# Kernel optimization log

Hardware: AMD Instinct MI355X
Metric: run time of the kernel (lower is better)

## Reference

```python
import jax, jax.numpy as jnp
import numpy as np

N = 50000
E = 800000
IN_C, HID_C, OUT_C = 128, 128, 64


def setup_inputs() -> dict:
    key = jax.random.key(0)
    k1, k2, k3, k4 = jax.random.split(key, 4)
    x = jax.random.normal(k1, (N, IN_C), dtype=jnp.float32)
    edge_index = jax.random.randint(k2, (2, E), 0, N, dtype=jnp.int32)
    # Glorot-ish init for the two linear layers (PyG GCNConv uses glorot)
    W1 = jax.random.normal(k3, (IN_C, HID_C), dtype=jnp.float32) / np.sqrt(IN_C)
    b1 = jnp.zeros((HID_C,), dtype=jnp.float32)
    W2 = jax.random.normal(k4, (HID_C, OUT_C), dtype=jnp.float32) / np.sqrt(HID_C)
    b2 = jnp.zeros((OUT_C,), dtype=jnp.float32)
    return {"x": x, "edge_index": edge_index, "W1": W1, "b1": b1, "W2": W2, "b2": b2}


def _gcn_norm(edge_index, num_nodes):
    # Add self-loops, then symmetric normalization deg^{-1/2}[row]*deg^{-1/2}[col]
    loop = jnp.arange(num_nodes, dtype=edge_index.dtype)
    row = jnp.concatenate([edge_index[0], loop])  # [E+N] source
    col = jnp.concatenate([edge_index[1], loop])  # [E+N] destination
    deg = jax.ops.segment_sum(jnp.ones_like(col, dtype=jnp.float32), col,
                              num_segments=num_nodes)
    deg_isqrt = jax.lax.rsqrt(deg)  # deg >= 1 due to self-loops
    norm = deg_isqrt[row] * deg_isqrt[col]  # [E+N]
    return row, col, norm


def _gcn_conv(x, row, col, norm, W, b, num_nodes):
    x = x @ W                                   # [N, C_out]
    msg = x[row] * norm[:, None]                # gather + scale, [E+N, C_out]
    out = jax.ops.segment_sum(msg, col, num_segments=num_nodes)  # scatter-add
    return out + b


def reference(x, edge_index, W1, b1, W2, b2):
    num_nodes = x.shape[0]
    row, col, norm = _gcn_norm(edge_index, num_nodes)
    h = _gcn_conv(x, row, col, norm, W1, b1, num_nodes)
    h = jax.nn.relu(h)
    out = _gcn_conv(h, row, col, norm, W2, b2, num_nodes)
    return out
```

## Files before the change

kernel.cpp:

```cpp
#include <hip/hip_runtime.h>


typedef float f32x4 __attribute__((ext_vector_type(4)));
typedef short bf16x8 __attribute__((ext_vector_type(8)));

#define EPB 4096

__device__ inline float bf2f(unsigned short u) {
    return __uint_as_float(((unsigned int)u) << 16);
}
__device__ inline unsigned short f2bf(float f) {
    unsigned int x = __float_as_uint(f);
    x = x + 0x7FFFu + ((x >> 16) & 1u);
    return (unsigned short)(x >> 16);
}
__device__ inline float4 cvt4(ushort4 u) {
    return make_float4(bf2f(u.x), bf2f(u.y), bf2f(u.z), bf2f(u.w));
}

__global__ __launch_bounds__(256) void k_rhist(const int* __restrict__ col,
                                               int* __restrict__ bbase,
                                               int* __restrict__ bucket_cnt,
                                               const float* __restrict__ W1,
                                               const float* __restrict__ W2,
                                               unsigned short* __restrict__ Wt1,
                                               unsigned short* __restrict__ Wt2,
                                               int e, int nbR, int nbB) {
    if ((int)blockIdx.x >= nbR) {
        int i = ((int)blockIdx.x - nbR) * 256 + threadIdx.x;
        if (i < 16384) {
            int k = i >> 7, nc = i & 127;
            Wt1[nc * 128 + k] = f2bf(W1[i]);
        } else if (i < 24576) {
            int i2 = i - 16384;
            int k = i2 >> 6, nc = i2 & 63;
            Wt2[nc * 128 + k] = f2bf(W2[i2]);
        }
        return;
    }
    __shared__ int h[256];
    int t = threadIdx.x;
    h[t] = 0;
    __syncthreads();
    int base = blockIdx.x * EPB;
#pragma unroll
    for (int i = 0; i < EPB / 256; ++i) {
        int idx = base + t + i * 256;
        if (idx < e) atomicAdd(&h[col[idx] >> 8], 1);
    }
    __syncthreads();
    if (t < nbB) bbase[t * nbR + blockIdx.x] = atomicAdd(&bucket_cnt[t], h[t]);
}

__global__ __launch_bounds__(256) void k_scanB(const int* __restrict__ bucket_cnt,
                                               int* __restrict__ bucket_base, int nbB) {
    __shared__ int s[256];
    int t = threadIdx.x;
    int v = (t < nbB) ? bucket_cnt[t] : 0;
    s[t] = v;
    __syncthreads();
#pragma unroll
    for (int off = 1; off < 256; off <<= 1) {
        int u = (t >= off) ? s[t - off] : 0;
        __syncthreads();
        s[t] += u;
        __syncthreads();
    }
    if (t < nbB) bucket_base[t] = s[t] - v;
    if (t == 255) bucket_base[nbB] = s[255];
}

__global__ __launch_bounds__(256) void k_rscatter(const int* __restrict__ row,
                                                  const int* __restrict__ col,
                                                  const int* __restrict__ bucket_base,
                                                  const int* __restrict__ bbase,
                                                  unsigned int* __restrict__ tmp,
                                                  int e, int nbR, int nbB) {
    __shared__ int base[256];
    __shared__ int h[256];
    int t = threadIdx.x;
    base[t] = (t < nbB) ? bucket_base[t] + bbase[t * nbR + blockIdx.x] : 0;
    h[t] = 0;
    __syncthreads();
    int b0 = blockIdx.x * EPB;
#pragma unroll
    for (int i = 0; i < EPB / 256; ++i) {
        int idx = b0 + t + i * 256;
        if (idx < e) {
            int c = col[idx];
            int bin = c >> 8;
            int rk = atomicAdd(&h[bin], 1);
            tmp[base[bin] + rk] =
                ((unsigned int)(c & 255) << 16) | (unsigned int)row[idx];
        }
    }
}

__global__ __launch_bounds__(256) void k_bsort(const unsigned int* __restrict__ tmp,
                                               const int* __restrict__ bucket_base,
                                               int* __restrict__ indptr,
                                               float* __restrict__ dinv,
                                               unsigned short* __restrict__ srcidx,
                                               int n, int e, int nbB) {
    __shared__ int cnt[256];
    __shared__ int pre[256];
    int b = blockIdx.x;
    int t = threadIdx.x;
    int beg = bucket_base[b];
    int end = bucket_base[b + 1];

    cnt[t] = 0;
    __syncthreads();
    for (int i = beg + t; i < end; i += 256) atomicAdd(&cnt[tmp[i] >> 16], 1);
    __syncthreads();
    int v = cnt[t];
    pre[t] = v;
    __syncthreads();
#pragma unroll
    for (int off = 1; off < 256; off <<= 1) {
        int u = (t >= off) ? pre[t - off] : 0;
        __syncthreads();
        pre[t] += u;
        __syncthreads();
    }
    int myexcl = pre[t] - v;
    int node = b * 256 + t;
    if (node < n) {
        indptr[node] = beg + myexcl;
        dinv[node] = rsqrtf((float)v + 1.0f);
    }
    if (b == nbB - 1 && t == 0) indptr[n] = e;
    __syncthreads();
    pre[t] = beg + myexcl;
    cnt[t] = 0;
    __syncthreads();
    for (int i = beg + t; i < end; i += 256) {
        unsigned int u = tmp[i];
        int cl = u >> 16;
        int rk = atomicAdd(&cnt[cl], 1);
        srcidx[pre[cl] + rk] = (unsigned short)(u & 0xFFFFu);
    }
}

__global__ __launch_bounds__(256, 2) void k_gemm1(const float* __restrict__ x,
                                                  const unsigned short* __restrict__ Wt,
                                                  const float* __restrict__ dinv,
                                                  unsigned short* __restrict__ hs, int n) {
    __shared__ unsigned short Xs[128 * 136];
    __shared__ unsigned short Ws[128 * 136];
    __shared__ float dinv_s[128];
    int t = threadIdx.x;
    int r0blk = blockIdx.x * 128;

#pragma unroll
    for (int i = 0; i < 8; ++i) {
        int c = t + i * 256;
        int nc = c >> 4;
        int k0 = (c & 15) * 8;
        bf16x8 v = *(const bf16x8*)&Wt[nc * 128 + k0];
        *(bf16x8*)&Ws[nc * 136 + k0] = v;
    }
#pragma unroll
    for (int i = 0; i < 16; ++i) {
        int c = t + i * 256;
        int r = c >> 5;
        int kq = c & 31;
        float4 v = make_float4(0.f, 0.f, 0.f, 0.f);
        int gr = r0blk + r;
        if (gr < n) v = ((const float4*)x)[gr * 32 + kq];
        ushort4 o;
        o.x = f2bf(v.x); o.y = f2bf(v.y); o.z = f2bf(v.z); o.w = f2bf(v.w);
        *(ushort4*)&Xs[r * 136 + kq * 4] = o;
    }
    if (t < 128) {
        int gr = r0blk + t;
        dinv_s[t] = (gr < n) ? dinv[gr] : 0.f;
    }
    __syncthreads();

    int lane = t & 63, wave = t >> 6;
    int lrow = lane & 15;
    int lk = (lane >> 4) * 8;

    f32x4 acc[2][8];
#pragma unroll
    for (int mi = 0; mi < 2; ++mi)
#pragma unroll
        for (int ni = 0; ni < 8; ++ni) acc[mi][ni] = (f32x4){0.f, 0.f, 0.f, 0.f};

#pragma unroll
    for (int ks = 0; ks < 4; ++ks) {
        int kk = ks * 32 + lk;
        bf16x8 a0 = *(bf16x8*)&Xs[(wave * 32 + lrow) * 136 + kk];
        bf16x8 a1 = *(bf16x8*)&Xs[(wave * 32 + 16 + lrow) * 136 + kk];
#pragma unroll
        for (int ni = 0; ni < 8; ++ni) {
            bf16x8 b = *(bf16x8*)&Ws[(ni * 16 + lrow) * 136 + kk];
            acc[0][ni] = __builtin_amdgcn_mfma_f32_16x16x32_bf16(a0, b, acc[0][ni], 0, 0, 0);
            acc[1][ni] = __builtin_amdgcn_mfma_f32_16x16x32_bf16(a1, b, acc[1][ni], 0, 0, 0);
        }
    }

    int rq = (lane >> 4) * 4;
#pragma unroll
    for (int mi = 0; mi < 2; ++mi)
#pragma unroll
        for (int r = 0; r < 4; ++r) {
            int lrw = wave * 32 + mi * 16 + rq + r;
            int grow = r0blk + lrw;
            if (grow < n) {
                float dv = dinv_s[lrw];
#pragma unroll
                for (int ni = 0; ni < 8; ++ni)
                    hs[grow * 128 + ni * 16 + lrow] = f2bf(acc[mi][ni][r] * dv);
            }
        }
}

__global__ __launch_bounds__(256) void k_gather1(const int* __restrict__ indptr,
                                                 const unsigned short* __restrict__ srcidx,
                                                 const unsigned short* __restrict__ hs,
                                                 const float* __restrict__ dinv,
                                                 const float* __restrict__ b1,
                                                 unsigned short* __restrict__ h1, int n) {
    int wid = (blockIdx.x * 256 + threadIdx.x) >> 6;
    if (wid >= n) return;
    int lane = threadIdx.x & 63;
    int half = lane >> 5;
    int hl = lane & 31;
    const ushort4* hv = (const ushort4*)hs;

    int beg = indptr[wid], end = indptr[wid + 1];
    float4 a0 = make_float4(0.f, 0.f, 0.f, 0.f), a1 = a0, a2 = a0, a3 = a0;

    int j = beg;
    for (; j + 7 < end; j += 8) {
        int sA = srcidx[j + half];
        int sB = srcidx[j + 2 + half];
        int sC = srcidx[j + 4 + half];
        int sD = srcidx[j + 6 + half];
        float4 v;
        v = cvt4(hv[sA * 32 + hl]); a0.x += v.x; a0.y += v.y; a0.z += v.z; a0.w += v.w;
        v = cvt4(hv[sB * 32 + hl]); a1.x += v.x; a1.y += v.y; a1.z += v.z; a1.w += v.w;
        v = cvt4(hv[sC * 32 + hl]); a2.x += v.x; a2.y += v.y; a2.z += v.z; a2.w += v.w;
        v = cvt4(hv[sD * 32 + hl]); a3.x += v.x; a3.y += v.y; a3.z += v.z; a3.w += v.w;
    }
    if (j + half < end) {
        float4 v = cvt4(hv[srcidx[j + half] * 32 + hl]);
        a0.x += v.x; a0.y += v.y; a0.z += v.z; a0.w += v.w;
    }
    j += 2;
    if (j + half < end) {
        float4 v = cvt4(hv[srcidx[j + half] * 32 + hl]);
        a1.x += v.x; a1.y += v.y; a1.z += v.z; a1.w += v.w;
    }
    j += 2;
    if (j + half < end) {
        float4 v = cvt4(hv[srcidx[j + half] * 32 + hl]);
        a2.x += v.x; a2.y += v.y; a2.z += v.z; a2.w += v.w;
    }
    j += 2;
    if (j + half < end) {
        float4 v = cvt4(hv[srcidx[j + half] * 32 + hl]);
        a3.x += v.x; a3.y += v.y; a3.z += v.z; a3.w += v.w;
    }

    float4 sv = cvt4(hv[wid * 32 + hl]);
    if (half == 0) {
        a0.x += sv.x; a0.y += sv.y; a0.z += sv.z; a0.w += sv.w;
    }

    float4 tsum;
    tsum.x = a0.x + a1.x + a2.x + a3.x;
    tsum.y = a0.y + a1.y + a2.y + a3.y;
    tsum.z = a0.z + a1.z + a2.z + a3.z;
    tsum.w = a0.w + a1.w + a2.w + a3.w;
    tsum.x += __shfl_xor(tsum.x, 32);
    tsum.y += __shfl_xor(tsum.y, 32);
    tsum.z += __shfl_xor(tsum.z, 32);
    tsum.w += __shfl_xor(tsum.w, 32);

    if (half == 0) {
        float d = dinv[wid];
        float4 bb = *(const float4*)&b1[hl * 4];
        ushort4 o;
        o.x = f2bf(fmaxf(tsum.x * d + bb.x, 0.f));
        o.y = f2bf(fmaxf(tsum.y * d + bb.y, 0.f));
        o.z = f2bf(fmaxf(tsum.z * d + bb.z, 0.f));
        o.w = f2bf(fmaxf(tsum.w * d + bb.w, 0.f));
        ((ushort4*)h1)[wid * 32 + hl] = o;
    }
}

__global__ __launch_bounds__(256, 3) void k_gemm2(const unsigned short* __restrict__ h1,
                                                  const unsigned short* __restrict__ Wt,
                                                  const float* __restrict__ dinv,
                                                  unsigned short* __restrict__ ps2, int n) {
    __shared__ unsigned short Xs[128 * 136];
    __shared__ unsigned short Ws[64 * 136];
    __shared__ float dinv_s[128];
    int t = threadIdx.x;
    int r0blk = blockIdx.x * 128;

#pragma unroll
    for (int i = 0; i < 4; ++i) {
        int c = t + i * 256;
        int nc = c >> 4;
        int k0 = (c & 15) * 8;
        bf16x8 v = *(const bf16x8*)&Wt[nc * 128 + k0];
        *(bf16x8*)&Ws[nc * 136 + k0] = v;
    }
#pragma unroll
    for (int i = 0; i < 8; ++i) {
        int c = t + i * 256;
        int r = c >> 4;
        int k0 = (c & 15) * 8;
        int gr = r0blk + r;
        bf16x8 v = (bf16x8)(short)0;
        if (gr < n) v = *(const bf16x8*)&h1[gr * 128 + k0];
        *(bf16x8*)&Xs[r * 136 + k0] = v;
    }
    if (t < 128) {
        int gr = r0blk + t;
        dinv_s[t] = (gr < n) ? dinv[gr] : 0.f;
    }
    __syncthreads();

    int lane = t & 63, wave = t >> 6;
    int lrow = lane & 15;
    int lk = (lane >> 4) * 8;

    f32x4 acc[2][4];
#pragma unroll
    for (int mi = 0; mi < 2; ++mi)
#pragma unroll
        for (int ni = 0; ni < 4; ++ni) acc[mi][ni] = (f32x4){0.f, 0.f, 0.f, 0.f};

#pragma unroll
    for (int ks = 0; ks < 4; ++ks) {
        int kk = ks * 32 + lk;
        bf16x8 a0 = *(bf16x8*)&Xs[(wave * 32 + lrow) * 136 + kk];
        bf16x8 a1 = *(bf16x8*)&Xs[(wave * 32 + 16 + lrow) * 136 + kk];
#pragma unroll
        for (int ni = 0; ni < 4; ++ni) {
            bf16x8 b = *(bf16x8*)&Ws[(ni * 16 + lrow) * 136 + kk];
            acc[0][ni] = __builtin_amdgcn_mfma_f32_16x16x32_bf16(a0, b, acc[0][ni], 0, 0, 0);
            acc[1][ni] = __builtin_amdgcn_mfma_f32_16x16x32_bf16(a1, b, acc[1][ni], 0, 0, 0);
        }
    }

    int rq = (lane >> 4) * 4;
#pragma unroll
    for (int mi = 0; mi < 2; ++mi)
#pragma unroll
        for (int r = 0; r < 4; ++r) {
            int lrw = wave * 32 + mi * 16 + rq + r;
            int grow = r0blk + lrw;
            if (grow < n) {
                float dv = dinv_s[lrw];
#pragma unroll
                for (int ni = 0; ni < 4; ++ni)
                    ps2[grow * 64 + ni * 16 + lrow] = f2bf(acc[mi][ni][r] * dv);
            }
        }
}

__global__ __launch_bounds__(256) void k_gather2(const int* __restrict__ indptr,
                                                 const unsigned short* __restrict__ srcidx,
                                                 const unsigned short* __restrict__ ps2,
                                                 const float* __restrict__ dinv,
                                                 const float* __restrict__ b2,
                                                 float* __restrict__ out, int n) {
    int wid = (blockIdx.x * 256 + threadIdx.x) >> 6;
    if (wid >= n) return;
    int lane = threadIdx.x & 63;
    int half = lane >> 5;
    int hl = lane & 31;
    const unsigned int* pv = (const unsigned int*)ps2;

    int beg = indptr[wid], end = indptr[wid + 1];
    float2 a0 = make_float2(0.f, 0.f), a1 = a0, a2 = a0, a3 = a0;

    int j = beg;
    for (; j + 7 < end; j += 8) {
        int sA = srcidx[j + half];
        int sB = srcidx[j + 2 + half];
        int sC = srcidx[j + 4 + half];
        int sD = srcidx[j + 6 + half];
        unsigned int uA = pv[sA * 32 + hl];
        unsigned int uB = pv[sB * 32 + hl];
        unsigned int uC = pv[sC * 32 + hl];
        unsigned int uD = pv[sD * 32 + hl];
        a0.x += bf2f((unsigned short)uA); a0.y += bf2f((unsigned short)(uA >> 16));
        a1.x += bf2f((unsigned short)uB); a1.y += bf2f((unsigned short)(uB >> 16));
        a2.x += bf2f((unsigned short)uC); a2.y += bf2f((unsigned short)(uC >> 16));
        a3.x += bf2f((unsigned short)uD); a3.y += bf2f((unsigned short)(uD >> 16));
    }
    if (j + half < end) {
        unsigned int u = pv[srcidx[j + half] * 32 + hl];
        a0.x += bf2f((unsigned short)u); a0.y += bf2f((unsigned short)(u >> 16));
    }
    j += 2;
    if (j + half < end) {
        unsigned int u = pv[srcidx[j + half] * 32 + hl];
        a1.x += bf2f((unsigned short)u); a1.y += bf2f((unsigned short)(u >> 16));
    }
    j += 2;
    if (j + half < end) {
        unsigned int u = pv[srcidx[j + half] * 32 + hl];
        a2.x += bf2f((unsigned short)u); a2.y += bf2f((unsigned short)(u >> 16));
    }
    j += 2;
    if (j + half < end) {
        unsigned int u = pv[srcidx[j + half] * 32 + hl];
        a3.x += bf2f((unsigned short)u); a3.y += bf2f((unsigned short)(u >> 16));
    }

    unsigned int us = pv[wid * 32 + hl];
    if (half == 0) {
        a0.x += bf2f((unsigned short)us); a0.y += bf2f((unsigned short)(us >> 16));
    }

    float2 tsum;
    tsum.x = a0.x + a1.x + a2.x + a3.x;
    tsum.y = a0.y + a1.y + a2.y + a3.y;
    tsum.x += __shfl_xor(tsum.x, 32);
    tsum.y += __shfl_xor(tsum.y, 32);

    if (half == 0) {
        float d = dinv[wid];
        float2 bb = *(const float2*)&b2[hl * 2];
        float2 o;
        o.x = tsum.x * d + bb.x;
        o.y = tsum.y * d + bb.y;
        ((float2*)out)[wid * 32 + hl] = o;
    }
}

extern "C" void kernel_launch(void* const* d_in, const int* in_sizes, int n_in,
                              void* d_out, int out_size, void* d_ws, size_t ws_size,
                              hipStream_t stream) {
    const float* x  = (const float*)d_in[0];
    const int*   ei = (const int*)d_in[1];
    const float* W1 = (const float*)d_in[2];
    const float* b1 = (const float*)d_in[3];
    const float* W2 = (const float*)d_in[4];
    const float* b2 = (const float*)d_in[5];
    float* out = (float*)d_out;

    int n = in_sizes[0] / 128;
    int e = in_sizes[1] / 2;
    const int* row = ei;
    const int* col = ei + e;

    int nbR = (e + EPB - 1) / EPB;
    int nbB = (n + 255) / 256;
    int m   = nbB * nbR;

    int* iw = (int*)d_ws;
    size_t o = 0;
    int* bucket_cnt  = iw + o; o += 256;
    int* bucket_base = iw + o; o += 256;
    int* bbase       = iw + o; o += (size_t)m;           o = (o + 3) & ~(size_t)3;
    int* indptr      = iw + o; o += (size_t)(n + 1);     o = (o + 3) & ~(size_t)3;
    float* dinv      = (float*)(iw + o); o += (size_t)n; o = (o + 3) & ~(size_t)3;
    unsigned int* tmp = (unsigned int*)(iw + o); o += (size_t)e; o = (o + 3) & ~(size_t)3;
    unsigned short* srcidx = (unsigned short*)(iw + o); o += (size_t)(e / 2 + 2); o = (o + 3) & ~(size_t)3;
    unsigned short* Wt1 = (unsigned short*)(iw + o); o += 8192;
    unsigned short* Wt2 = (unsigned short*)(iw + o); o += 4096;
    unsigned short* hs  = (unsigned short*)(iw + o);
    unsigned short* h1  = hs + (size_t)n * 128;
    unsigned short* ps2 = hs;

    hipMemsetAsync(bucket_cnt, 0, 256 * sizeof(int), stream);
    k_rhist<<<nbR + 96, 256, 0, stream>>>(col, bbase, bucket_cnt, W1, W2, Wt1, Wt2, e, nbR, nbB);
    k_scanB<<<1, 256, 0, stream>>>(bucket_cnt, bucket_base, nbB);
    k_rscatter<<<nbR, 256, 0, stream>>>(row, col, bucket_base, bbase, tmp, e, nbR, nbB);
    k_bsort<<<nbB, 256, 0, stream>>>(tmp, bucket_base, indptr, dinv, srcidx, n, e, nbB);

    int nbg = (n + 127) / 128;
    k_gemm1<<<nbg, 256, 0, stream>>>(x, Wt1, dinv, hs, n);
    k_gather1<<<(n * 64 + 255) / 256, 256, 0, stream>>>(indptr, srcidx, hs, dinv, b1, h1, n);
    k_gemm2<<<nbg, 256, 0, stream>>>(h1, Wt2, dinv, ps2, n);
    k_gather2<<<(n * 64 + 255) / 256, 256, 0, stream>>>(indptr, srcidx, ps2, dinv, b2, out, n);
}
```

Measured before the change: 136.5 us.

## Fold bucket scan into scatter/sort kernels and split gather edges contiguously per half-wave

```diff
diff --git a/kernel.cpp b/kernel.cpp
--- a/kernel.cpp
+++ b/kernel.cpp
@@ -16,6 +16,9 @@
 }
 __device__ inline float4 cvt4(ushort4 u) {
     return make_float4(bf2f(u.x), bf2f(u.y), bf2f(u.z), bf2f(u.w));
+}
+__device__ inline void add4(float4& a, float4 v) {
+    a.x += v.x; a.y += v.y; a.z += v.z; a.w += v.w;
 }
 
 __global__ __launch_bounds__(256) void k_rhist(const int* __restrict__ col,
@@ -52,34 +55,27 @@
     if (t < nbB) bbase[t * nbR + blockIdx.x] = atomicAdd(&bucket_cnt[t], h[t]);
 }
 
-__global__ __launch_bounds__(256) void k_scanB(const int* __restrict__ bucket_cnt,
-                                               int* __restrict__ bucket_base, int nbB) {
-    __shared__ int s[256];
-    int t = threadIdx.x;
-    int v = (t < nbB) ? bucket_cnt[t] : 0;
-    s[t] = v;
-    __syncthreads();
-#pragma unroll
-    for (int off = 1; off < 256; off <<= 1) {
-        int u = (t >= off) ? s[t - off] : 0;
-        __syncthreads();
-        s[t] += u;
-        __syncthreads();
-    }
-    if (t < nbB) bucket_base[t] = s[t] - v;
-    if (t == 255) bucket_base[nbB] = s[255];
-}
-
 __global__ __launch_bounds__(256) void k_rscatter(const int* __restrict__ row,
                                                   const int* __restrict__ col,
-                                                  const int* __restrict__ bucket_base,
+                                                  const int* __restrict__ bucket_cnt,
                                                   const int* __restrict__ bbase,
                                                   unsigned int* __restrict__ tmp,
                                                   int e, int nbR, int nbB) {
     __shared__ int base[256];
     __shared__ int h[256];
     int t = threadIdx.x;
-    base[t] = (t < nbB) ? bucket_base[t] + bbase[t * nbR + blockIdx.x] : 0;
+    int v = (t < nbB) ? bucket_cnt[t] : 0;
+    base[t] = v;
+    __syncthreads();
+#pragma unroll
+    for (int off = 1; off < 256; off <<= 1) {
+        int u = (t >= off) ? base[t - off] : 0;
+        __syncthreads();
+        base[t] += u;
+        __syncthreads();
+    }
+    int excl = base[t] - v;
+    base[t] = excl + ((t < nbB) ? bbase[t * nbR + blockIdx.x] : 0);
     h[t] = 0;
     __syncthreads();
     int b0 = blockIdx.x * EPB;
@@ -97,7 +93,7 @@
 }
 
 __global__ __launch_bounds__(256) void k_bsort(const unsigned int* __restrict__ tmp,
-                                               const int* __restrict__ bucket_base,
+                                               const int* __restrict__ bucket_cnt,
                                                int* __restrict__ indptr,
                                                float* __restrict__ dinv,
                                                unsigned short* __restrict__ srcidx,
@@ -106,14 +102,26 @@
     __shared__ int pre[256];
     int b = blockIdx.x;
     int t = threadIdx.x;
-    int beg = bucket_base[b];
-    int end = bucket_base[b + 1];
+
+    int v = (t < nbB) ? bucket_cnt[t] : 0;
+    pre[t] = v;
+    __syncthreads();
+#pragma unroll
+    for (int off = 1; off < 256; off <<= 1) {
+        int u = (t >= off) ? pre[t - off] : 0;
+        __syncthreads();
+        pre[t] += u;
+        __syncthreads();
+    }
+    int beg = pre[b] - ((b < nbB) ? bucket_cnt[b] : 0);
+    int end = pre[b];
+    __syncthreads();
 
     cnt[t] = 0;
     __syncthreads();
     for (int i = beg + t; i < end; i += 256) atomicAdd(&cnt[tmp[i] >> 16], 1);
     __syncthreads();
-    int v = cnt[t];
+    v = cnt[t];
     pre[t] = v;
     __syncthreads();
 #pragma unroll
@@ -231,44 +239,39 @@
     const ushort4* hv = (const ushort4*)hs;
 
     int beg = indptr[wid], end = indptr[wid + 1];
+    int c0 = (end - beg + 1) >> 1;
+    int j    = beg + half * c0;
+    int jend = half ? end : (beg + c0);
+
     float4 a0 = make_float4(0.f, 0.f, 0.f, 0.f), a1 = a0, a2 = a0, a3 = a0;
 
-    int j = beg;
-    for (; j + 7 < end; j += 8) {
-        int sA = srcidx[j + half];
-        int sB = srcidx[j + 2 + half];
-        int sC = srcidx[j + 4 + half];
-        int sD = srcidx[j + 6 + half];
-        float4 v;
-        v = cvt4(hv[sA * 32 + hl]); a0.x += v.x; a0.y += v.y; a0.z += v.z; a0.w += v.w;
-        v = cvt4(hv[sB * 32 + hl]); a1.x += v.x; a1.y += v.y; a1.z += v.z; a1.w += v.w;
-        v = cvt4(hv[sC * 32 + hl]); a2.x += v.x; a2.y += v.y; a2.z += v.z; a2.w += v.w;
-        v = cvt4(hv[sD * 32 + hl]); a3.x += v.x; a3.y += v.y; a3.z += v.z; a3.w += v.w;
-    }
-    if (j + half < end) {
-        float4 v = cvt4(hv[srcidx[j + half] * 32 + hl]);
-        a0.x += v.x; a0.y += v.y; a0.z += v.z; a0.w += v.w;
-    }
-    j += 2;
-    if (j + half < end) {
-        float4 v = cvt4(hv[srcidx[j + half] * 32 + hl]);
-        a1.x += v.x; a1.y += v.y; a1.z += v.z; a1.w += v.w;
-    }
-    j += 2;
-    if (j + half < end) {
-        float4 v = cvt4(hv[srcidx[j + half] * 32 + hl]);
-        a2.x += v.x; a2.y += v.y; a2.z += v.z; a2.w += v.w;
-    }
-    j += 2;
-    if (j + half < end) {
-        float4 v = cvt4(hv[srcidx[j + half] * 32 + hl]);
-        a3.x += v.x; a3.y += v.y; a3.z += v.z; a3.w += v.w;
-    }
-
-    float4 sv = cvt4(hv[wid * 32 + hl]);
-    if (half == 0) {
-        a0.x += sv.x; a0.y += sv.y; a0.z += sv.z; a0.w += sv.w;
-    }
+    for (; j + 7 < jend; j += 8) {
+        int s0 = srcidx[j],     s1 = srcidx[j + 1];
+        int s2 = srcidx[j + 2], s3 = srcidx[j + 3];
+        int s4 = srcidx[j + 4], s5 = srcidx[j + 5];
+        int s6 = srcidx[j + 6], s7 = srcidx[j + 7];
+        float4 v0 = cvt4(hv[s0 * 32 + hl]);
+        float4 v1 = cvt4(hv[s1 * 32 + hl]);
+        float4 v2 = cvt4(hv[s2 * 32 + hl]);
+        float4 v3 = cvt4(hv[s3 * 32 + hl]);
+        float4 v4 = cvt4(hv[s4 * 32 + hl]);
+        float4 v5 = cvt4(hv[s5 * 32 + hl]);
+        float4 v6 = cvt4(hv[s6 * 32 + hl]);
+        float4 v7 = cvt4(hv[s7 * 32 + hl]);
+        add4(a0, v0); add4(a1, v1); add4(a2, v2); add4(a3, v3);
+        add4(a0, v4); add4(a1, v5); add4(a2, v6); add4(a3, v7);
+    }
+    if (j + 3 < jend) {
+        int s0 = srcidx[j], s1 = srcidx[j + 1], s2 = srcidx[j + 2], s3 = srcidx[j + 3];
+        add4(a0, cvt4(hv[s0 * 32 + hl]));
+        add4(a1, cvt4(hv[s1 * 32 + hl]));
+        add4(a2, cvt4(hv[s2 * 32 + hl]));
+        add4(a3, cvt4(hv[s3 * 32 + hl]));
+        j += 4;
+    }
+    for (; j < jend; ++j) add4(a0, cvt4(hv[srcidx[j] * 32 + hl]));
+
+    if (half == 0) add4(a1, cvt4(hv[wid * 32 + hl]));
 
     float4 tsum;
     tsum.x = a0.x + a1.x + a2.x + a3.x;
@@ -379,46 +382,54 @@
     const unsigned int* pv = (const unsigned int*)ps2;
 
     int beg = indptr[wid], end = indptr[wid + 1];
+    int c0 = (end - beg + 1) >> 1;
+    int j    = beg + half * c0;
+    int jend = half ? end : (beg + c0);
+
     float2 a0 = make_float2(0.f, 0.f), a1 = a0, a2 = a0, a3 = a0;
 
-    int j = beg;
-    for (; j + 7 < end; j += 8) {
-        int sA = srcidx[j + half];
-        int sB = srcidx[j + 2 + half];
-        int sC = srcidx[j + 4 + half];
-        int sD = srcidx[j + 6 + half];
-        unsigned int uA = pv[sA * 32 + hl];
-        unsigned int uB = pv[sB * 32 + hl];
-        unsigned int uC = pv[sC * 32 + hl];
-        unsigned int uD = pv[sD * 32 + hl];
-        a0.x += bf2f((unsigned short)uA); a0.y += bf2f((unsigned short)(uA >> 16));
-        a1.x += bf2f((unsigned short)uB); a1.y += bf2f((unsigned short)(uB >> 16));
-        a2.x += bf2f((unsigned short)uC); a2.y += bf2f((unsigned short)(uC >> 16));
-        a3.x += bf2f((unsigned short)uD); a3.y += bf2f((unsigned short)(uD >> 16));
-    }
-    if (j + half < end) {
-        unsigned int u = pv[srcidx[j + half] * 32 + hl];
+    for (; j + 7 < jend; j += 8) {
+        int s0 = srcidx[j],     s1 = srcidx[j + 1];
+        int s2 = srcidx[j + 2], s3 = srcidx[j + 3];
+        int s4 = srcidx[j + 4], s5 = srcidx[j + 5];
+        int s6 = srcidx[j + 6], s7 = srcidx[j + 7];
+        unsigned int u0 = pv[s0 * 32 + hl];
+        unsigned int u1 = pv[s1 * 32 + hl];
+        unsigned int u2 = pv[s2 * 32 + hl];
+        unsigned int u3 = pv[s3 * 32 + hl];
+        unsigned int u4 = pv[s4 * 32 + hl];
+        unsigned int u5 = pv[s5 * 32 + hl];
+        unsigned int u6 = pv[s6 * 32 + hl];
+        unsigned int u7 = pv[s7 * 32 + hl];
+        a0.x += bf2f((unsigned short)u0); a0.y += bf2f((unsigned short)(u0 >> 16));
+        a1.x += bf2f((unsigned short)u1); a1.y += bf2f((unsigned short)(u1 >> 16));
+        a2.x += bf2f((unsigned short)u2); a2.y += bf2f((unsigned short)(u2 >> 16));
+        a3.x += bf2f((unsigned short)u3); a3.y += bf2f((unsigned short)(u3 >> 16));
+        a0.x += bf2f((unsigned short)u4); a0.y += bf2f((unsigned short)(u4 >> 16));
+        a1.x += bf2f((unsigned short)u5); a1.y += bf2f((unsigned short)(u5 >> 16));
+        a2.x += bf2f((unsigned short)u6); a2.y += bf2f((unsigned short)(u6 >> 16));
+        a3.x += bf2f((unsigned short)u7); a3.y += bf2f((unsigned short)(u7 >> 16));
+    }
+    if (j + 3 < jend) {
+        int s0 = srcidx[j], s1 = srcidx[j + 1], s2 = srcidx[j + 2], s3 = srcidx[j + 3];
+        unsigned int u0 = pv[s0 * 32 + hl];
+        unsigned int u1 = pv[s1 * 32 + hl];
+        unsigned int u2 = pv[s2 * 32 + hl];
+        unsigned int u3 = pv[s3 * 32 + hl];
+        a0.x += bf2f((unsigned short)u0); a0.y += bf2f((unsigned short)(u0 >> 16));
+        a1.x += bf2f((unsigned short)u1); a1.y += bf2f((unsigned short)(u1 >> 16));
+        a2.x += bf2f((unsigned short)u2); a2.y += bf2f((unsigned short)(u2 >> 16));
+        a3.x += bf2f((unsigned short)u3); a3.y += bf2f((unsigned short)(u3 >> 16));
+        j += 4;
+    }
+    for (; j < jend; ++j) {
+        unsigned int u = pv[srcidx[j] * 32 + hl];
         a0.x += bf2f((unsigned short)u); a0.y += bf2f((unsigned short)(u >> 16));
     }
-    j += 2;
-    if (j + half < end) {
-        unsigned int u = pv[srcidx[j + half] * 32 + hl];
+
+    if (half == 0) {
+        unsigned int u = pv[wid * 32 + hl];
         a1.x += bf2f((unsigned short)u); a1.y += bf2f((unsigned short)(u >> 16));
-    }
-    j += 2;
-    if (j + half < end) {
-        unsigned int u = pv[srcidx[j + half] * 32 + hl];
-        a2.x += bf2f((unsigned short)u); a2.y += bf2f((unsigned short)(u >> 16));
-    }
-    j += 2;
-    if (j + half < end) {
-        unsigned int u = pv[srcidx[j + half] * 32 + hl];
-        a3.x += bf2f((unsigned short)u); a3.y += bf2f((unsigned short)(u >> 16));
-    }
-
-    unsigned int us = pv[wid * 32 + hl];
-    if (half == 0) {
-        a0.x += bf2f((unsigned short)us); a0.y += bf2f((unsigned short)(us >> 16));
     }
 
     float2 tsum;
@@ -460,7 +471,6 @@
     int* iw = (int*)d_ws;
     size_t o = 0;
     int* bucket_cnt  = iw + o; o += 256;
-    int* bucket_base = iw + o; o += 256;
     int* bbase       = iw + o; o += (size_t)m;           o = (o + 3) & ~(size_t)3;
     int* indptr      = iw + o; o += (size_t)(n + 1);     o = (o + 3) & ~(size_t)3;
     float* dinv      = (float*)(iw + o); o += (size_t)n; o = (o + 3) & ~(size_t)3;
@@ -474,9 +484,8 @@
 
     hipMemsetAsync(bucket_cnt, 0, 256 * sizeof(int), stream);
     k_rhist<<<nbR + 96, 256, 0, stream>>>(col, bbase, bucket_cnt, W1, W2, Wt1, Wt2, e, nbR, nbB);
-    k_scanB<<<1, 256, 0, stream>>>(bucket_cnt, bucket_base, nbB);
-    k_rscatter<<<nbR, 256, 0, stream>>>(row, col, bucket_base, bbase, tmp, e, nbR, nbB);
-    k_bsort<<<nbB, 256, 0, stream>>>(tmp, bucket_base, indptr, dinv, srcidx, n, e, nbB);
+    k_rscatter<<<nbR, 256, 0, stream>>>(row, col, bucket_cnt, bbase, tmp, e, nbR, nbB);
+    k_bsort<<<nbB, 256, 0, stream>>>(tmp, bucket_cnt, indptr, dinv, srcidx, n, e, nbB);
 
     int nbg = (n + 127) / 128;
     k_gemm1<<<nbg, 256, 0, stream>>>(x, Wt1, dinv, hs, n);
```

Result: no change. 136.4 us (-0.1%).
